# Performance work log

Hardware: AMD Instinct MI355X
Metric: run time of the kernel (lower is better)

## Reference

```python
import jax, jax.numpy as jnp
import numpy as np

N, HID, HEADS = 50000, 256, 8
D = HID // HEADS  # per-head dim = 32
E = 800000


def setup_inputs() -> dict:
    key = jax.random.key(0)
    ks = jax.random.split(key, 12)
    s = 0.02
    x = jax.random.normal(ks[0], (N, HID), dtype=jnp.float32)
    edge_index = jax.random.randint(ks[1], (2, E), 0, N, dtype=jnp.int64)
    # TransformerConv params (PyG defaults: root_weight=True, concat=True, beta=False)
    Wq = jax.random.normal(ks[2], (HID, HID), dtype=jnp.float32) * s
    bq = jnp.zeros((HID,), dtype=jnp.float32)
    Wk = jax.random.normal(ks[3], (HID, HID), dtype=jnp.float32) * s
    bk = jnp.zeros((HID,), dtype=jnp.float32)
    Wv = jax.random.normal(ks[4], (HID, HID), dtype=jnp.float32) * s
    bv = jnp.zeros((HID,), dtype=jnp.float32)
    Wskip = jax.random.normal(ks[5], (HID, HID), dtype=jnp.float32) * s
    bskip = jnp.zeros((HID,), dtype=jnp.float32)
    gamma = jnp.ones((HID,), dtype=jnp.float32)
    beta = jnp.zeros((HID,), dtype=jnp.float32)
    return {"x": x, "edge_index": edge_index, "Wq": Wq, "bq": bq, "Wk": Wk,
            "bk": bk, "Wv": Wv, "bv": bv, "Wskip": Wskip, "bskip": bskip,
            "gamma": gamma, "beta": beta}


def _gnn_layer(x, edge_index, Wq, bq, Wk, bk, Wv, bv, Wskip, bskip, gamma, beta):
    n = x.shape[0]
    src, dst = edge_index[0], edge_index[1]  # messages flow src(j) -> dst(i)
    q = (x @ Wq + bq).reshape(n, HEADS, D)
    k = (x @ Wk + bk).reshape(n, HEADS, D)
    v = (x @ Wv + bv).reshape(n, HEADS, D)
    # per-edge attention logits [E, HEADS]
    logits = jnp.einsum('ehd,ehd->eh', q[dst], k[src]) / jnp.sqrt(jnp.float32(D))
    # segment softmax over destination neighborhoods (stable)
    seg_max = jax.ops.segment_max(logits, dst, num_segments=n)  # [N, HEADS]
    expv = jnp.exp(logits - seg_max[dst])
    denom = jax.ops.segment_sum(expv, dst, num_segments=n)
    attn = expv / denom[dst]  # [E, HEADS]  (dropout in eval mode -> identity)
    # scatter-aggregate weighted values, concat heads
    agg = jax.ops.segment_sum(attn[:, :, None] * v[src], dst, num_segments=n)
    out = agg.reshape(n, HID) + (x @ Wskip + bskip)  # root/skip connection
    h = jax.nn.gelu(out, approximate=False)
    # residual + LayerNorm
    y = x + h
    mu = jnp.mean(y, axis=-1, keepdims=True)
    var = jnp.var(y, axis=-1, keepdims=True)
    return (y - mu) / jnp.sqrt(var + 1e-5) * gamma + beta


def reference(x, edge_index, Wq, bq, Wk, bk, Wv, bv, Wskip, bskip, gamma, beta):
    return _gnn_layer(x, edge_index, Wq, bq, Wk, bk, Wv, bv, Wskip, bskip, gamma, beta)
```

## Files before the change

kernel.cpp:

```cpp
#include <hip/hip_runtime.h>

#define N_NODES 50000
#define HID 256
#define HEADS 8
#define HDIM 32
#define N_EDGES 800000

typedef __bf16 bf16x8 __attribute__((ext_vector_type(8)));
typedef float f32x4 __attribute__((ext_vector_type(4)));
typedef float f32x2 __attribute__((ext_vector_type(2)));

__device__ __forceinline__ unsigned short f2bf(float f) {
    unsigned int b = __float_as_uint(f);
    unsigned int r = (b + 0x7FFFu + ((b >> 16) & 1u)) >> 16;
    return (unsigned short)r;
}
__device__ __forceinline__ float bf2f(unsigned short u) {
    return __uint_as_float(((unsigned int)u) << 16);
}
__device__ __forceinline__ f32x2 bfpair(unsigned int u) {
    f32x2 r;
    r[0] = __uint_as_float(u << 16);
    r[1] = __uint_as_float(u & 0xffff0000u);
    return r;
}

__device__ __forceinline__ void fused_col_map(int p, int& mat, int& col, float& scale) {
    if (p < 256) { mat = 0; col = p; scale = 1.0f; }
    else if (p < 768) {
        int pp = p - 256;
        mat = ((pp & 2) ? 2 : 1);
        col = ((pp >> 2) << 1) | (pp & 1);
        scale = 64.0f;
    } else { mat = 3; col = p - 768; scale = 1.0f; }
}

__global__ __launch_bounds__(256) void prep_kernel(
    const float* __restrict__ x, unsigned short* __restrict__ xb,
    const int* __restrict__ dst, int* __restrict__ deg,
    const float* __restrict__ Wq, const float* __restrict__ Wk,
    const float* __restrict__ Wv, const float* __restrict__ Ws,
    const float* __restrict__ bq, const float* __restrict__ bk,
    const float* __restrict__ bv, const float* __restrict__ bs,
    unsigned short* __restrict__ wpack, float* __restrict__ biasF) {
    int b = blockIdx.x;
    if (b < 6250) {
        int t = b * 256 + threadIdx.x;
        const float4* p = reinterpret_cast<const float4*>(x) + (size_t)t * 2;
        float4 f0 = p[0], f1 = p[1];
        uint4 o;
        o.x = (unsigned)f2bf(f0.x) | ((unsigned)f2bf(f0.y) << 16);
        o.y = (unsigned)f2bf(f0.z) | ((unsigned)f2bf(f0.w) << 16);
        o.z = (unsigned)f2bf(f1.x) | ((unsigned)f2bf(f1.y) << 16);
        o.w = (unsigned)f2bf(f1.z) | ((unsigned)f2bf(f1.w) << 16);
        reinterpret_cast<uint4*>(xb)[t] = o;
    } else if (b < 9375) {
        int e = (b - 6250) * 256 + threadIdx.x;
        atomicAdd(&deg[dst[e]], 1);
    } else {
        int t = (b - 9375) * 256 + threadIdx.x;
        int e = t & 7, lane = (t >> 3) & 63, kk = (t >> 9) & 7, n_tile = t >> 12;
        int k = kk * 32 + (lane >> 4) * 8 + e;
        int p = n_tile * 16 + (lane & 15);
        const float* W[4] = {Wq, Wk, Wv, Ws};
        int mat, col; float scale;
        fused_col_map(p, mat, col, scale);
        wpack[t] = f2bf(W[mat][k * 256 + col] * scale);
        if (t < 1024) {
            const float* B[4] = {bq, bk, bv, bs};
            int mat2, col2; float s2;
            fused_col_map(t, mat2, col2, s2);
            biasF[t] = B[mat2][col2] * s2;
        }
    }
}

__global__ __launch_bounds__(1024) void scan1_kernel(
    const int* __restrict__ deg, int* __restrict__ row_ptr,
    int* __restrict__ btot, int n) {
    int tid = threadIdx.x, lane = tid & 63, wv = tid >> 6;
    int idx = blockIdx.x * 1024 + tid;
    int v = (idx < n) ? deg[idx] : 0;
    int inc = v;
#pragma unroll
    for (int off = 1; off < 64; off <<= 1) {
        int t2 = __shfl_up(inc, off);
        if (lane >= off) inc += t2;
    }
    __shared__ int sW[16], sO[16];
    if (lane == 63) sW[wv] = inc;
    __syncthreads();
    if (tid < 16) {
        int vv = sW[tid], in2 = vv;
        for (int off = 1; off < 16; off <<= 1) {
            int t2 = __shfl_up(in2, off);
            if (tid >= off) in2 += t2;
        }
        sO[tid] = in2 - vv;
    }
    __syncthreads();
    int excl = sO[wv] + inc - v;
    if (idx <= n) row_ptr[idx] = excl;
    if (tid == 1023) btot[blockIdx.x] = excl + v;
}

__global__ __launch_bounds__(256) void fixup_kernel(
    int* __restrict__ row_ptr, int* __restrict__ fill,
    const int* __restrict__ btot, int n) {
    __shared__ int sB;
    int tid = threadIdx.x;
    if (tid < 64) {
        int v = (tid < 50) ? btot[tid] : 0;
        int inc = v;
#pragma unroll
        for (int off = 1; off < 64; off <<= 1) {
            int t2 = __shfl_up(inc, off);
            if (tid >= off) inc += t2;
        }
        if (tid == (blockIdx.x >> 2)) sB = inc - v;
    }
    __syncthreads();
    int idx = blockIdx.x * 256 + tid;
    if (idx > n) return;
    int v = row_ptr[idx] + sB;
    row_ptr[idx] = v;
    if (idx < n) fill[idx] = v;
}

__global__ __launch_bounds__(256) void gemm_scatter_kernel(
    const int* __restrict__ src, const int* __restrict__ dst,
    int* __restrict__ fill, unsigned short* __restrict__ csr_src,
    const unsigned short* __restrict__ xb,
    const unsigned short* __restrict__ wpack,
    const float* __restrict__ biasF,
    unsigned short* __restrict__ qs,
    unsigned char* __restrict__ kv,
    unsigned short* __restrict__ sk,
    int n_nodes) {
    __shared__ __align__(16) uint4 bsh[2048];
    int b = blockIdx.x;
    if (b >= 6256) {
        int e = (b - 6256) * 256 + threadIdx.x;
        if (e < N_EDGES) {
            int pos = atomicAdd(&fill[dst[e]], 1);
            csr_src[pos] = (unsigned short)src[e];
        }
        return;
    }
    int work = (b & 7) * 782 + (b >> 3);
    int mt = work >> 4;
    int nt = work & 15;
    int lane = threadIdx.x & 63;
    int wv = threadIdx.x >> 6;
    int row_w = mt * 128 + wv * 32;
    int n0 = nt * 64;
    int ntile0 = n0 >> 4;

    {
        const uint4* bsrc = reinterpret_cast<const uint4*>(wpack) +
                            (size_t)ntile0 * 8 * 64;
        int tid = threadIdx.x;
#pragma unroll
        for (int i = 0; i < 8; ++i)
            bsh[i * 256 + tid] = bsrc[i * 256 + tid];
    }
    __syncthreads();

    f32x4 acc[2][4];
#pragma unroll
    for (int mi = 0; mi < 2; ++mi)
#pragma unroll
        for (int ni = 0; ni < 4; ++ni) {
            f32x4 z = {0.f, 0.f, 0.f, 0.f};
            acc[mi][ni] = z;
        }

    int arow0 = min(row_w + (lane & 15), n_nodes - 1);
    int arow1 = min(row_w + 16 + (lane & 15), n_nodes - 1);
    int acol = (lane >> 4) * 8;

#pragma unroll
    for (int kk = 0; kk < 8; ++kk) {
        bf16x8 a[2], bfr[4];
        {
            uint4 u0 = *reinterpret_cast<const uint4*>(xb + (size_t)arow0 * 256 + kk * 32 + acol);
            uint4 u1 = *reinterpret_cast<const uint4*>(xb + (size_t)arow1 * 256 + kk * 32 + acol);
            a[0] = __builtin_bit_cast(bf16x8, u0);
            a[1] = __builtin_bit_cast(bf16x8, u1);
        }
#pragma unroll
        for (int ni = 0; ni < 4; ++ni) {
            uint4 u = bsh[(ni * 8 + kk) * 64 + lane];
            bfr[ni] = __builtin_bit_cast(bf16x8, u);
        }
#pragma unroll
        for (int mi = 0; mi < 2; ++mi)
#pragma unroll
            for (int ni = 0; ni < 4; ++ni)
                acc[mi][ni] = __builtin_amdgcn_mfma_f32_16x16x32_bf16(
                    a[mi], bfr[ni], acc[mi][ni], 0, 0, 0);
    }

    int region = (n0 < 256) ? 0 : (n0 < 768 ? 1 : 2);
#pragma unroll
    for (int mi = 0; mi < 2; ++mi) {
        int rbase = row_w + mi * 16 + (lane >> 4) * 4;
#pragma unroll
        for (int ni = 0; ni < 4; ++ni) {
            int col = n0 + ni * 16 + (lane & 15);
            float bias = biasF[col];
#pragma unroll
            for (int r = 0; r < 4; ++r) {
                int row = rbase + r;
                if (row < n_nodes) {
                    float val = acc[mi][ni][r] + bias;
                    if (region == 0) {
                        qs[(size_t)row * 256 + col] = f2bf(val);
                    } else if (region == 1) {
                        int p8 = __builtin_amdgcn_cvt_pk_fp8_f32(val, val, 0, false);
                        kv[(size_t)row * 512 + (col - 256)] = (unsigned char)(p8 & 0xff);
                    } else {
                        sk[(size_t)row * 256 + (col - 768)] = f2bf(val);
                    }
                }
            }
        }
    }
}

__global__ __launch_bounds__(256) void edge_agg_kernel(
    const int* __restrict__ row_ptr, const unsigned short* __restrict__ csr_src,
    const unsigned short* __restrict__ qs, const unsigned char* __restrict__ kv,
    const unsigned short* __restrict__ sk, const unsigned short* __restrict__ xb,
    const float* __restrict__ gamma, const float* __restrict__ beta,
    float* __restrict__ out) {
    int wv = threadIdx.x >> 6;
    int i = blockIdx.x * 4 + wv;
    int lane = threadIdx.x & 63;
    int half = lane >> 5, l = lane & 31;

    const float QS = 0.17677669529663687f * 1.4426950408889634f / 64.0f;
    uint4 qu = *reinterpret_cast<const uint4*>(qs + (size_t)i * 256 + l * 8);
    f32x2 qsc = {QS, QS};
    f32x2 q01 = bfpair(qu.x) * qsc;
    f32x2 q23 = bfpair(qu.y) * qsc;
    f32x2 q45 = bfpair(qu.z) * qsc;
    f32x2 q67 = bfpair(qu.w) * qsc;

    int e0 = row_ptr[i], e1 = row_ptr[i + 1];
    f32x2 acc0 = {0.f, 0.f}, acc1 = {0.f, 0.f}, acc2 = {0.f, 0.f}, acc3 = {0.f, 0.f};
    float den = 0.f;
    int e = e0 + half;
    int j = (e < e1) ? (int)csr_src[e] : 0;
    while (e < e1) {
        int jn = (e + 2 < e1) ? (int)csr_src[e + 2] : 0;
        uint4 u = *reinterpret_cast<const uint4*>(
            kv + (size_t)j * 512u + (unsigned)l * 16u);
        f32x2 k01 = __builtin_amdgcn_cvt_pk_f32_fp8(u.x, false);
        f32x2 v01 = __builtin_amdgcn_cvt_pk_f32_fp8(u.x, true);
        f32x2 k23 = __builtin_amdgcn_cvt_pk_f32_fp8(u.y, false);
        f32x2 v23 = __builtin_amdgcn_cvt_pk_f32_fp8(u.y, true);
        f32x2 k45 = __builtin_amdgcn_cvt_pk_f32_fp8(u.z, false);
        f32x2 v45 = __builtin_amdgcn_cvt_pk_f32_fp8(u.z, true);
        f32x2 k67 = __builtin_amdgcn_cvt_pk_f32_fp8(u.w, false);
        f32x2 v67 = __builtin_amdgcn_cvt_pk_f32_fp8(u.w, true);
        f32x2 d = q01 * k01;
        d = __builtin_elementwise_fma(q23, k23, d);
        d = __builtin_elementwise_fma(q45, k45, d);
        d = __builtin_elementwise_fma(q67, k67, d);
        float s = d[0] + d[1];
        s += __shfl_xor(s, 1);
        s += __shfl_xor(s, 2);
        float w = exp2f(s);
        den += w;
        f32x2 w2 = {w, w};
        acc0 = __builtin_elementwise_fma(w2, v01, acc0);
        acc1 = __builtin_elementwise_fma(w2, v23, acc1);
        acc2 = __builtin_elementwise_fma(w2, v45, acc2);
        acc3 = __builtin_elementwise_fma(w2, v67, acc3);
        j = jn;
        e += 2;
    }

    acc0[0] += __shfl_xor(acc0[0], 32); acc0[1] += __shfl_xor(acc0[1], 32);
    acc1[0] += __shfl_xor(acc1[0], 32); acc1[1] += __shfl_xor(acc1[1], 32);
    acc2[0] += __shfl_xor(acc2[0], 32); acc2[1] += __shfl_xor(acc2[1], 32);
    acc3[0] += __shfl_xor(acc3[0], 32); acc3[1] += __shfl_xor(acc3[1], 32);
    den += __shfl_xor(den, 32);
    float inv = (den > 0.f) ? 1.0f / (den * 64.0f) : 0.f;

    uint4 su = *reinterpret_cast<const uint4*>(sk + (size_t)i * 256 + l * 8);
    uint4 xu = *reinterpret_cast<const uint4*>(xb + (size_t)i * 256 + l * 8);
    const float C1 = -2.3022650556f;
    const float C2 = -0.10294578f;
    float s1 = 0.f, s2 = 0.f;
    f32x2 y01, y23, y45, y67;
#define GNN_PROC(A, SRAW, XRAW, Y)                                   \
    {                                                                \
        f32x2 skp = bfpair(SRAW), xr = bfpair(XRAW);                 \
        _Pragma("unroll")                                            \
        for (int qq = 0; qq < 2; ++qq) {                             \
            float pre = fmaf(A[qq], inv, skp[qq]);                   \
            float x2 = pre * pre;                                    \
            float arg = pre * fmaf(C2, x2, C1);                      \
            float gel = pre / (1.f + exp2f(arg));                    \
            float yy = xr[qq] + gel;                                 \
            Y[qq] = yy;                                              \
            s1 += yy;                                                \
            s2 = fmaf(yy, yy, s2);                                   \
        }                                                            \
    }
    GNN_PROC(acc0, su.x, xu.x, y01)
    GNN_PROC(acc1, su.y, xu.y, y23)
    GNN_PROC(acc2, su.z, xu.z, y45)
    GNN_PROC(acc3, su.w, xu.w, y67)
#undef GNN_PROC

#pragma unroll
    for (int m = 1; m <= 16; m <<= 1) {
        s1 += __shfl_xor(s1, m);
        s2 += __shfl_xor(s2, m);
    }
    float mu = s1 * (1.f / 256.f);
    float var = s2 * (1.f / 256.f) - mu * mu;
    float rstd = rsqrtf(var + 1e-5f);

    if (half == 0) {
        const float4* g4 = reinterpret_cast<const float4*>(gamma) + l * 2;
        const float4* b4 = reinterpret_cast<const float4*>(beta) + l * 2;
        float4 ga = g4[0], gb = g4[1], ba = b4[0], bb = b4[1];
        float4 o0, o1;
        o0.x = (y01[0] - mu) * rstd * ga.x + ba.x;
        o0.y = (y01[1] - mu) * rstd * ga.y + ba.y;
        o0.z = (y23[0] - mu) * rstd * ga.z + ba.z;
        o0.w = (y23[1] - mu) * rstd * ga.w + ba.w;
        o1.x = (y45[0] - mu) * rstd * gb.x + bb.x;
        o1.y = (y45[1] - mu) * rstd * gb.y + bb.y;
        o1.z = (y67[0] - mu) * rstd * gb.z + bb.z;
        o1.w = (y67[1] - mu) * rstd * gb.w + bb.w;
        float4* op = reinterpret_cast<float4*>(out + (size_t)i * 256 + l * 8);
        op[0] = o0;
        op[1] = o1;
    }
}

extern "C" void kernel_launch(void* const* d_in, const int* in_sizes, int n_in,
                              void* d_out, int out_size, void* d_ws, size_t ws_size,
                              hipStream_t stream) {
    const float* x    = (const float*)d_in[0];
    const int*   ei   = (const int*)d_in[1];
    const float* Wq   = (const float*)d_in[2];
    const float* bq   = (const float*)d_in[3];
    const float* Wk   = (const float*)d_in[4];
    const float* bk   = (const float*)d_in[5];
    const float* Wv   = (const float*)d_in[6];
    const float* bv   = (const float*)d_in[7];
    const float* Wsk  = (const float*)d_in[8];
    const float* bsk  = (const float*)d_in[9];
    const float* gamma = (const float*)d_in[10];
    const float* beta  = (const float*)d_in[11];
    const int* src = ei;
    const int* dst = ei + N_EDGES;

    char* ws = (char*)d_ws;
    size_t off = 0;
    auto alloc = [&](size_t bytes) -> void* {
        void* p = ws + off;
        off += (bytes + 255) & ~(size_t)255;
        return p;
    };
    unsigned short* xb     = (unsigned short*)alloc((size_t)N_NODES * 256 * 2);
    unsigned short* qs     = (unsigned short*)alloc((size_t)N_NODES * 256 * 2);
    unsigned char*  kvb    = (unsigned char*)alloc((size_t)N_NODES * 512);
    unsigned short* sk     = (unsigned short*)alloc((size_t)N_NODES * 256 * 2);
    unsigned short* wpack  = (unsigned short*)alloc(262144 * 2);
    float*          biasF  = (float*)alloc(1024 * 4);
    int*            deg    = (int*)alloc((size_t)N_NODES * 4);
    int*            rowp   = (int*)alloc((size_t)(N_NODES + 1) * 4);
    int*            fill   = (int*)alloc((size_t)N_NODES * 4);
    unsigned short* csr    = (unsigned short*)alloc((size_t)N_EDGES * 2);
    int*            btot   = (int*)alloc(64 * 4);
    (void)ws_size;

    hipMemsetAsync(deg, 0, (size_t)N_NODES * 4, stream);
    prep_kernel<<<10399, 256, 0, stream>>>(x, xb, dst, deg, Wq, Wk, Wv, Wsk,
                                           bq, bk, bv, bsk, wpack, biasF);
    scan1_kernel<<<50, 1024, 0, stream>>>(deg, rowp, btot, N_NODES);
    fixup_kernel<<<196, 256, 0, stream>>>(rowp, fill, btot, N_NODES);
    gemm_scatter_kernel<<<9381, 256, 0, stream>>>(src, dst, fill, csr,
                                                  xb, wpack, biasF, qs, kvb, sk, N_NODES);
    edge_agg_kernel<<<12500, 256, 0, stream>>>(rowp, csr, qs, kvb, sk, xb, gamma, beta,
                                               (float*)d_out);
}
```

Measured before the change: 268.5 us.

## Double GEMM M-tile, interleave scatter blocks, unroll edge loop by two

The GEMM blocks now compute 256 rows instead of 128, with four 16-row MFMA subtiles per wave. This halves how often the shared-memory weight tile is reloaded and halves the GEMM block count. The CSR scatter blocks are interleaved with GEMM blocks (odd block ids) rather than appended at the end, so the atomic scatter overlaps the compute. The edge aggregation loop handles two edges per half-wave per iteration, issuing two KV gathers together to raise memory-level parallelism. The costs are higher register pressure from 64 accumulators and more divergent tail handling.

```diff
diff --git a/kernel.cpp b/kernel.cpp
--- a/kernel.cpp
+++ b/kernel.cpp
@@ -138,21 +138,23 @@
     unsigned short* __restrict__ sk,
     int n_nodes) {
     __shared__ __align__(16) uint4 bsh[2048];
-    int b = blockIdx.x;
-    if (b >= 6256) {
-        int e = (b - 6256) * 256 + threadIdx.x;
-        if (e < N_EDGES) {
+    int bid = blockIdx.x;
+    if (bid & 1) {
+        int sid = bid >> 1;
+        int e = sid * 256 + threadIdx.x;
+        if (sid < 3125 && e < N_EDGES) {
             int pos = atomicAdd(&fill[dst[e]], 1);
             csr_src[pos] = (unsigned short)src[e];
         }
         return;
     }
-    int work = (b & 7) * 782 + (b >> 3);
+    int gid = bid >> 1;
+    int work = (gid & 7) * 392 + (gid >> 3);
     int mt = work >> 4;
     int nt = work & 15;
     int lane = threadIdx.x & 63;
     int wv = threadIdx.x >> 6;
-    int row_w = mt * 128 + wv * 32;
+    int row_w = mt * 256 + wv * 32;
     int n0 = nt * 64;
     int ntile0 = n0 >> 4;
 
@@ -166,27 +168,30 @@
     }
     __syncthreads();
 
-    f32x4 acc[2][4];
-#pragma unroll
-    for (int mi = 0; mi < 2; ++mi)
+    f32x4 acc[4][4];
+#pragma unroll
+    for (int ms = 0; ms < 4; ++ms)
 #pragma unroll
         for (int ni = 0; ni < 4; ++ni) {
             f32x4 z = {0.f, 0.f, 0.f, 0.f};
-            acc[mi][ni] = z;
-        }
-
-    int arow0 = min(row_w + (lane & 15), n_nodes - 1);
-    int arow1 = min(row_w + 16 + (lane & 15), n_nodes - 1);
+            acc[ms][ni] = z;
+        }
+
+    int arow[4];
+#pragma unroll
+    for (int ms = 0; ms < 4; ++ms)
+        arow[ms] = min(row_w + (ms & 1) * 16 + (ms >> 1) * 128 + (lane & 15),
+                       n_nodes - 1);
     int acol = (lane >> 4) * 8;
 
 #pragma unroll
     for (int kk = 0; kk < 8; ++kk) {
-        bf16x8 a[2], bfr[4];
-        {
-            uint4 u0 = *reinterpret_cast<const uint4*>(xb + (size_t)arow0 * 256 + kk * 32 + acol);
-            uint4 u1 = *reinterpret_cast<const uint4*>(xb + (size_t)arow1 * 256 + kk * 32 + acol);
-            a[0] = __builtin_bit_cast(bf16x8, u0);
-            a[1] = __builtin_bit_cast(bf16x8, u1);
+        bf16x8 a[4], bfr[4];
+#pragma unroll
+        for (int ms = 0; ms < 4; ++ms) {
+            uint4 u = *reinterpret_cast<const uint4*>(
+                xb + (size_t)arow[ms] * 256 + kk * 32 + acol);
+            a[ms] = __builtin_bit_cast(bf16x8, u);
         }
 #pragma unroll
         for (int ni = 0; ni < 4; ++ni) {
@@ -194,17 +199,17 @@
             bfr[ni] = __builtin_bit_cast(bf16x8, u);
         }
 #pragma unroll
-        for (int mi = 0; mi < 2; ++mi)
+        for (int ms = 0; ms < 4; ++ms)
 #pragma unroll
             for (int ni = 0; ni < 4; ++ni)
-                acc[mi][ni] = __builtin_amdgcn_mfma_f32_16x16x32_bf16(
-                    a[mi], bfr[ni], acc[mi][ni], 0, 0, 0);
+                acc[ms][ni] = __builtin_amdgcn_mfma_f32_16x16x32_bf16(
+                    a[ms], bfr[ni], acc[ms][ni], 0, 0, 0);
     }
 
     int region = (n0 < 256) ? 0 : (n0 < 768 ? 1 : 2);
 #pragma unroll
-    for (int mi = 0; mi < 2; ++mi) {
-        int rbase = row_w + mi * 16 + (lane >> 4) * 4;
+    for (int ms = 0; ms < 4; ++ms) {
+        int rbase = row_w + (ms & 1) * 16 + (ms >> 1) * 128 + (lane >> 4) * 4;
 #pragma unroll
         for (int ni = 0; ni < 4; ++ni) {
             int col = n0 + ni * 16 + (lane & 15);
@@ -213,7 +218,7 @@
             for (int r = 0; r < 4; ++r) {
                 int row = rbase + r;
                 if (row < n_nodes) {
-                    float val = acc[mi][ni][r] + bias;
+                    float val = acc[ms][ni][r] + bias;
                     if (region == 0) {
                         qs[(size_t)row * 256 + col] = f2bf(val);
                     } else if (region == 1) {
@@ -250,37 +255,55 @@
     int e0 = row_ptr[i], e1 = row_ptr[i + 1];
     f32x2 acc0 = {0.f, 0.f}, acc1 = {0.f, 0.f}, acc2 = {0.f, 0.f}, acc3 = {0.f, 0.f};
     float den = 0.f;
+
+#define EDGE_PROC(U)                                                     \
+    {                                                                    \
+        f32x2 k01 = __builtin_amdgcn_cvt_pk_f32_fp8(U.x, false);         \
+        f32x2 v01 = __builtin_amdgcn_cvt_pk_f32_fp8(U.x, true);          \
+        f32x2 k23 = __builtin_amdgcn_cvt_pk_f32_fp8(U.y, false);         \
+        f32x2 v23 = __builtin_amdgcn_cvt_pk_f32_fp8(U.y, true);          \
+        f32x2 k45 = __builtin_amdgcn_cvt_pk_f32_fp8(U.z, false);         \
+        f32x2 v45 = __builtin_amdgcn_cvt_pk_f32_fp8(U.z, true);          \
+        f32x2 k67 = __builtin_amdgcn_cvt_pk_f32_fp8(U.w, false);         \
+        f32x2 v67 = __builtin_amdgcn_cvt_pk_f32_fp8(U.w, true);          \
+        f32x2 d = q01 * k01;                                             \
+        d = __builtin_elementwise_fma(q23, k23, d);                      \
+        d = __builtin_elementwise_fma(q45, k45, d);                      \
+        d = __builtin_elementwise_fma(q67, k67, d);                      \
+        float s = d[0] + d[1];                                           \
+        s += __shfl_xor(s, 1);                                           \
+        s += __shfl_xor(s, 2);                                           \
+        float w = exp2f(s);                                              \
+        den += w;                                                        \
+        f32x2 w2 = {w, w};                                               \
+        acc0 = __builtin_elementwise_fma(w2, v01, acc0);                 \
+        acc1 = __builtin_elementwise_fma(w2, v23, acc1);                 \
+        acc2 = __builtin_elementwise_fma(w2, v45, acc2);                 \
+        acc3 = __builtin_elementwise_fma(w2, v67, acc3);                 \
+    }
+
     int e = e0 + half;
-    int j = (e < e1) ? (int)csr_src[e] : 0;
-    while (e < e1) {
-        int jn = (e + 2 < e1) ? (int)csr_src[e + 2] : 0;
-        uint4 u = *reinterpret_cast<const uint4*>(
-            kv + (size_t)j * 512u + (unsigned)l * 16u);
-        f32x2 k01 = __builtin_amdgcn_cvt_pk_f32_fp8(u.x, false);
-        f32x2 v01 = __builtin_amdgcn_cvt_pk_f32_fp8(u.x, true);
-        f32x2 k23 = __builtin_amdgcn_cvt_pk_f32_fp8(u.y, false);
-        f32x2 v23 = __builtin_amdgcn_cvt_pk_f32_fp8(u.y, true);
-        f32x2 k45 = __builtin_amdgcn_cvt_pk_f32_fp8(u.z, false);
-        f32x2 v45 = __builtin_amdgcn_cvt_pk_f32_fp8(u.z, true);
-        f32x2 k67 = __builtin_amdgcn_cvt_pk_f32_fp8(u.w, false);
-        f32x2 v67 = __builtin_amdgcn_cvt_pk_f32_fp8(u.w, true);
-        f32x2 d = q01 * k01;
-        d = __builtin_elementwise_fma(q23, k23, d);
-        d = __builtin_elementwise_fma(q45, k45, d);
-        d = __builtin_elementwise_fma(q67, k67, d);
-        float s = d[0] + d[1];
-        s += __shfl_xor(s, 1);
-        s += __shfl_xor(s, 2);
-        float w = exp2f(s);
-        den += w;
-        f32x2 w2 = {w, w};
-        acc0 = __builtin_elementwise_fma(w2, v01, acc0);
-        acc1 = __builtin_elementwise_fma(w2, v23, acc1);
-        acc2 = __builtin_elementwise_fma(w2, v45, acc2);
-        acc3 = __builtin_elementwise_fma(w2, v67, acc3);
-        j = jn;
-        e += 2;
-    }
+    int j0 = (e < e1) ? (int)csr_src[e] : 0;
+    int j1 = (e + 2 < e1) ? (int)csr_src[e + 2] : 0;
+    while (e + 2 < e1) {
+        uint4 ua = *reinterpret_cast<const uint4*>(
+            kv + (size_t)j0 * 512u + (unsigned)l * 16u);
+        uint4 ub = *reinterpret_cast<const uint4*>(
+            kv + (size_t)j1 * 512u + (unsigned)l * 16u);
+        int jn0 = (e + 4 < e1) ? (int)csr_src[e + 4] : 0;
+        int jn1 = (e + 6 < e1) ? (int)csr_src[e + 6] : 0;
+        EDGE_PROC(ua)
+        EDGE_PROC(ub)
+        j0 = jn0;
+        j1 = jn1;
+        e += 4;
+    }
+    if (e < e1) {
+        uint4 ua = *reinterpret_cast<const uint4*>(
+            kv + (size_t)j0 * 512u + (unsigned)l * 16u);
+        EDGE_PROC(ua)
+    }
+#undef EDGE_PROC
 
     acc0[0] += __shfl_xor(acc0[0], 32); acc0[1] += __shfl_xor(acc0[1], 32);
     acc1[0] += __shfl_xor(acc1[0], 32); acc1[1] += __shfl_xor(acc1[1], 32);
@@ -387,7 +410,7 @@
                                            bq, bk, bv, bsk, wpack, biasF);
     scan1_kernel<<<50, 1024, 0, stream>>>(deg, rowp, btot, N_NODES);
     fixup_kernel<<<196, 256, 0, stream>>>(rowp, fill, btot, N_NODES);
-    gemm_scatter_kernel<<<9381, 256, 0, stream>>>(src, dst, fill, csr,
+    gemm_scatter_kernel<<<6272, 256, 0, stream>>>(src, dst, fill, csr,
                                                   xb, wpack, biasF, qs, kvb, sk, N_NODES);
     edge_agg_kernel<<<12500, 256, 0, stream>>>(rowp, csr, qs, kvb, sk, xb, gamma, beta,
                                                (float*)d_out);
```

Result: slower. 296.5 us (+10.4%).
